# Kernel tuning notes

Hardware: AMD Instinct MI355X
Metric: run time of the kernel (lower is better)

The kernel has to match this reference:

```python
import jax, jax.numpy as jnp
import numpy as np

B, S, D = 1, 2048, 1024
HEADS, HEAD_DIM = 16, 64
GRID = (8, 16, 16)      # frames, height, width; prod == S
WIN = (3, 5, 5)         # window_f, window_h, window_w
NEG = -1e9


def _window_mask_3d(frames, height, width, wf, wh, ww):
    """[S, S] bool mask: True where kv is inside the 3D local window of q."""
    idx = np.arange(frames * height * width)
    f = idx // (height * width)
    hw = idx % (height * width)
    h = hw // width
    w = hw % width
    mf = np.abs(f[:, None] - f[None, :]) <= wf // 2
    mh = np.abs(h[:, None] - h[None, :]) <= wh // 2
    mw = np.abs(w[:, None] - w[None, :]) <= ww // 2
    return jnp.asarray(mf & mh & mw)


def setup_inputs() -> dict:
    key = jax.random.key(0)
    ks = jax.random.split(key, 6)
    sd = 1.0 / np.sqrt(D)
    return {
        "hidden_states": jax.random.normal(ks[0], (B, S, D), jnp.float32),
        "Wq": jax.random.normal(ks[1], (D, D), jnp.float32) * sd,
        "Wk": jax.random.normal(ks[2], (D, D), jnp.float32) * sd,
        "Wv": jax.random.normal(ks[3], (D, D), jnp.float32) * sd,
        "Wo": jax.random.normal(ks[4], (D, D), jnp.float32) * sd,
        "bo": jnp.zeros((D,), jnp.float32),
        "frames": GRID[0], "height": GRID[1], "width": GRID[2],
        "wf": WIN[0], "wh": WIN[1], "ww": WIN[2],
    }


def reference(hidden_states, Wq, Wk, Wv, Wo, bo, frames, height, width, wf, wh, ww):
    b, s, d = hidden_states.shape
    hd = d // HEADS
    scale = 1.0 / np.sqrt(hd)

    # QKV projections (attn.to_q / to_k / to_v, bias=False), self-attention
    q = (hidden_states @ Wq).reshape(b, s, HEADS, hd).transpose(0, 2, 1, 3)
    k = (hidden_states @ Wk).reshape(b, s, HEADS, hd).transpose(0, 2, 1, 3)
    v = (hidden_states @ Wv).reshape(b, s, HEADS, hd).transpose(0, 2, 1, 3)

    mask = _window_mask_3d(frames, height, width, wf, wh, ww)  # [S, S] bool

    # SDPA with boolean attn_mask (window-based block-sparse pattern)
    scores = jnp.einsum("bhqd,bhkd->bhqk", q, k) * scale
    scores = jnp.where(mask[None, None], scores, NEG)
    attnw = jax.nn.softmax(scores, axis=-1)
    out = jnp.einsum("bhqk,bhkd->bhqd", attnw, v)

    out = out.transpose(0, 2, 1, 3).reshape(b, s, d)
    return out @ Wo + bo
```

## Files before the change

kernel.cpp:

```cpp
#include <hip/hip_runtime.h>
#include <hip/hip_bf16.h>
#include <hip/hip_fp16.h>

#define SEQ   2048
#define DIM   1024
#define NHEAD 16
#define HD    64
#define QSCALE 0.18033688011112042f

typedef _Float16 half8 __attribute__((ext_vector_type(8)));
typedef _Float16 half4 __attribute__((ext_vector_type(4)));
typedef float    floatx4 __attribute__((ext_vector_type(4)));

__device__ __forceinline__ void gload16(const void* g, void* l) {
    __builtin_amdgcn_global_load_lds(
        (const __attribute__((address_space(1))) unsigned int*)g,
        (__attribute__((address_space(3))) unsigned int*)l, 16, 0, 0);
}

#define VMCNT(n) asm volatile("s_waitcnt vmcnt(" #n ")" ::: "memory")
#define BAR()    __builtin_amdgcn_s_barrier()

__global__ __launch_bounds__(256) void prep(
        const float* __restrict__ H, _Float16* __restrict__ Hf,
        const float* __restrict__ W0, const float* __restrict__ W1,
        const float* __restrict__ W2, const float* __restrict__ W3,
        _Float16* __restrict__ T) {
    __shared__ float tile[64][65];
    int z = blockIdx.z;
    int t = threadIdx.x;
    if (z < 4) {
        const float* W = (z == 0) ? W0 : (z == 1) ? W1 : (z == 2) ? W2 : W3;
        _Float16* Tz = T + (size_t)z * (DIM * DIM);
        int bx = blockIdx.x * 64;
        int by = blockIdx.y * 64;
        #pragma unroll
        for (int i = 0; i < 4; i++) {
            int id = t + i * 256;
            int r = id >> 4;
            int c = (id & 15) * 4;
            float4 v = *reinterpret_cast<const float4*>(W + (size_t)(by + r) * DIM + bx + c);
            tile[r][c] = v.x; tile[r][c + 1] = v.y; tile[r][c + 2] = v.z; tile[r][c + 3] = v.w;
        }
        __syncthreads();
        #pragma unroll
        for (int i = 0; i < 2; i++) {
            int id = t + i * 256;
            int nr = id >> 3;
            int c8 = id & 7;
            half8 o;
            #pragma unroll
            for (int j = 0; j < 8; j++) o[j] = (_Float16)tile[c8 * 8 + j][nr];
            *reinterpret_cast<half8*>(Tz + (size_t)(bx + nr) * DIM + by + c8 * 8) = o;
        }
    } else {
        int wg = blockIdx.y * 16 + blockIdx.x;
        #pragma unroll
        for (int i = 0; i < 4; i++) {
            int base = ((wg * 4 + i) * 256 + t) * 8;
            float4 v0 = *reinterpret_cast<const float4*>(H + base);
            float4 v1 = *reinterpret_cast<const float4*>(H + base + 4);
            half8 o = { (_Float16)v0.x, (_Float16)v0.y, (_Float16)v0.z, (_Float16)v0.w,
                        (_Float16)v1.x, (_Float16)v1.y, (_Float16)v1.z, (_Float16)v1.w };
            *reinterpret_cast<half8*>(Hf + base) = o;
        }
    }
}

__device__ __forceinline__ void gemm_core(const _Float16* __restrict__ Ap,
                                          const _Float16* __restrict__ Bp,
                                          char* lds, floatx4 (&acc)[4][4]) {
    const int tid  = threadIdx.x;
    const int lane = tid & 63;
    const int wid  = tid >> 6;
    const int wr = wid >> 1, wc = wid & 1;
    const int r16 = lane & 15;
    const int kk  = (lane >> 4) * 8;

    const int srow = tid >> 2, scol = (tid & 3) * 8;
    const _Float16* As0 = Ap + (size_t)srow * DIM + scol;
    const _Float16* Bs0 = Bp + (size_t)srow * DIM + scol;

    auto stage = [&](int buf, int t) {
        char* Ad = lds + buf * 32768;
        char* Bd = Ad + 16384;
        int k0 = t * 64;
        #pragma unroll
        for (int i = 0; i < 4; i++) {
            int off = (i & 1) * 64 * DIM + (i >> 1) * 32 + k0;
            gload16(As0 + off, Ad + i * 4096 + wid * 1024);
            gload16(Bs0 + off, Bd + i * 4096 + wid * 1024);
        }
    };

    auto compute = [&](int buf) {
        char* Ad = lds + buf * 32768;
        char* Bd = Ad + 16384;
        #pragma unroll
        for (int ks = 0; ks < 2; ks++) {
            half8 a[4], b[4];
            #pragma unroll
            for (int m = 0; m < 4; m++)
                a[m] = *reinterpret_cast<half8*>(Ad + ks * 8192 + (wr * 64 + m * 16 + r16) * 64 + kk * 2);
            #pragma unroll
            for (int n = 0; n < 4; n++)
                b[n] = *reinterpret_cast<half8*>(Bd + ks * 8192 + (wc * 64 + n * 16 + r16) * 64 + kk * 2);
            #pragma unroll
            for (int m = 0; m < 4; m++)
                #pragma unroll
                for (int n = 0; n < 4; n++)
                    acc[m][n] = __builtin_amdgcn_mfma_f32_16x16x32_f16(a[m], b[n], acc[m][n], 0, 0, 0);
        }
    };

    stage(0, 0);
    stage(1, 1);
    #pragma unroll 1
    for (int t = 0; t < 14; t += 2) {
        VMCNT(8); BAR();
        compute(0);
        BAR();
        stage(0, t + 2);
        VMCNT(8); BAR();
        compute(1);
        BAR();
        stage(1, t + 3);
    }
    VMCNT(8); BAR();
    compute(0);
    BAR();
    VMCNT(0); BAR();
    compute(1);
}

__global__ __launch_bounds__(256) void gemm_qkv(
        const _Float16* __restrict__ Hf, const _Float16* __restrict__ Wt,
        _Float16* __restrict__ Qp, _Float16* __restrict__ Kp, _Float16* __restrict__ Vt) {
    __shared__ char lds[65536];
    floatx4 acc[4][4] = {};

    int lin = blockIdx.x + 16 * blockIdx.y + 128 * blockIdx.z;
    int swz = (lin & 7) * 48 + (lin >> 3);
    int z  = swz >> 7;
    int rem = swz & 127;
    int bx = rem & 15, by = rem >> 4;

    int tm, tn;
    const _Float16 *Ap, *Bp;
    if (z < 2) {
        tm = bx; tn = by;
        Ap = Hf + (size_t)tm * 128 * DIM;
        Bp = Wt + (size_t)z * DIM * DIM + (size_t)tn * 128 * DIM;
    } else {
        tm = bx & 7; tn = by * 2 + (bx >> 3);
        Ap = Wt + (size_t)2 * DIM * DIM + (size_t)tm * 128 * DIM;
        Bp = Hf + (size_t)tn * 128 * DIM;
    }
    gemm_core(Ap, Bp, lds, acc);

    int lane = threadIdx.x & 63, wid = threadIdx.x >> 6;
    int wr = wid >> 1, wc = wid & 1;
    float qs = (z == 0) ? QSCALE : 1.0f;
    _Float16* Oz = (z == 0) ? Qp : Kp;

    #pragma unroll
    for (int m = 0; m < 4; m++) {
        #pragma unroll
        for (int n = 0; n < 4; n++) {
            #pragma unroll
            for (int r = 0; r < 4; r++) {
                int row = tm * 128 + wr * 64 + m * 16 + (lane >> 4) * 4 + r;
                int col = tn * 128 + wc * 64 + n * 16 + (lane & 15);
                float v = acc[m][n][r];
                if (z < 2) {
                    int head = col >> 6;
                    Oz[(size_t)head * (SEQ * HD) + (size_t)row * HD + (col & 63)] = (_Float16)(v * qs);
                } else {
                    Vt[(size_t)row * SEQ + col] = (_Float16)v;
                }
            }
        }
    }
}

__global__ __launch_bounds__(256) void gemm_o(
        const _Float16* __restrict__ AO, const _Float16* __restrict__ WoT,
        const float* __restrict__ bias, float* __restrict__ out) {
    __shared__ char lds[65536];
    floatx4 acc[4][4] = {};

    int lin = blockIdx.x + 16 * blockIdx.y;
    int swz = (lin & 7) * 16 + (lin >> 3);
    int tm = swz & 15, tn = swz >> 4;

    gemm_core(AO + (size_t)tm * 128 * DIM, WoT + (size_t)tn * 128 * DIM, lds, acc);

    int lane = threadIdx.x & 63, wid = threadIdx.x >> 6;
    int wr = wid >> 1, wc = wid & 1;
    #pragma unroll
    for (int m = 0; m < 4; m++) {
        #pragma unroll
        for (int n = 0; n < 4; n++) {
            #pragma unroll
            for (int r = 0; r < 4; r++) {
                int row = tm * 128 + wr * 64 + m * 16 + (lane >> 4) * 4 + r;
                int col = tn * 128 + wc * 64 + n * 16 + (lane & 15);
                out[(size_t)row * DIM + col] = acc[m][n][r] + bias[col];
            }
        }
    }
}

__global__ __launch_bounds__(256) void attn_mfma(
        const _Float16* __restrict__ Q,
        const _Float16* __restrict__ K,
        const _Float16* __restrict__ Vt,
        _Float16* __restrict__ AO) {
    __shared__ char P_lds[4][16 * 640];

    int wid  = threadIdx.x >> 6;
    int lane = threadIdx.x & 63;
    int g    = lane >> 4;
    int ql   = lane & 15;

    int blk  = blockIdx.x;
    int sblk = (blk & 7) * 64 + (blk >> 3);
    int bid  = sblk * 4 + wid;
    int rid  = bid & 127;
    int head = bid >> 7;
    int f    = rid >> 4;
    int hq   = rid & 15;
    int s0   = rid << 4;

    const _Float16* Qh = Q  + (size_t)head * (SEQ * HD);
    const _Float16* Kh = K  + (size_t)head * (SEQ * HD);
    const _Float16* Vh = Vt + (size_t)head * (HD * SEQ);

    int f_start = min(max(f - 1, 0), 5);
    int h_start = min(max(hq - 2, 0), 10);

    bool wm[4];
    #pragma unroll
    for (int r = 0; r < 4; r++) {
        int wp = g * 4 + r;
        wm[r] = (wp - ql <= 2) && (ql - wp <= 2);
    }

    half8 qf[2];
    #pragma unroll
    for (int ks = 0; ks < 2; ks++)
        qf[ks] = *reinterpret_cast<const half8*>(Qh + (size_t)(s0 + ql) * HD + ks * 32 + g * 8);

    float lsum = 0.f;
    int swz = (ql & 7) << 4;

    #pragma unroll
    for (int fi = 0; fi < 3; fi++) {
        int fp = f_start + fi;
        bool fok = (fp - f <= 1) && (f - fp <= 1);
        int sbase = fp * 256 + h_start * 16;
        const _Float16* Kc = Kh + (size_t)sbase * HD;

        floatx4 sacc[6];
        #pragma unroll
        for (int j = 0; j < 6; j++) sacc[j] = (floatx4){0.f, 0.f, 0.f, 0.f};

        #pragma unroll
        for (int j = 0; j < 6; j++) {
            #pragma unroll
            for (int ks = 0; ks < 2; ks++) {
                half8 kf = *reinterpret_cast<const half8*>(Kc + (size_t)(j * 16 + ql) * HD + ks * 32 + g * 8);
                sacc[j] = __builtin_amdgcn_mfma_f32_16x16x32_f16(kf, qf[ks], sacc[j], 0, 0, 0);
            }
        }

        #pragma unroll
        for (int j = 0; j < 6; j++) {
            int hp = h_start + j;
            bool ok = fok && (hp - hq <= 2) && (hq - hp <= 2);
            half4 pv;
            #pragma unroll
            for (int r = 0; r < 4; r++) {
                float sv = (ok && wm[r]) ? sacc[j][r] : -10000.f;
                float p  = __builtin_amdgcn_exp2f(sv);
                lsum += p;
                pv[r] = (_Float16)p;
            }
            int byte = (ql * 640 + (fi * 96 + j * 16 + g * 4) * 2) ^ swz;
            *reinterpret_cast<half4*>(&P_lds[wid][byte]) = pv;
        }
    }

    lsum += __shfl_xor(lsum, 16);
    lsum += __shfl_xor(lsum, 32);
    float inv = __builtin_amdgcn_rcpf(lsum);

    __syncthreads();

    floatx4 oacc[4];
    #pragma unroll
    for (int dt = 0; dt < 4; dt++) oacc[dt] = (floatx4){0.f, 0.f, 0.f, 0.f};

    #pragma unroll
    for (int fi = 0; fi < 3; fi++) {
        int sbase = (f_start + fi) * 256 + h_start * 16;
        #pragma unroll
        for (int kw = 0; kw < 3; kw++) {
            int kcol = fi * 96 + kw * 32;
            int byte = (ql * 640 + (kcol + g * 8) * 2) ^ swz;
            half8 pa = *reinterpret_cast<half8*>(&P_lds[wid][byte]);
            #pragma unroll
            for (int dt = 0; dt < 4; dt++) {
                half8 vf = *reinterpret_cast<const half8*>(
                    Vh + (size_t)(dt * 16 + ql) * SEQ + sbase + kw * 32 + g * 8);
                oacc[dt] = __builtin_amdgcn_mfma_f32_16x16x32_f16(pa, vf, oacc[dt], 0, 0, 0);
            }
        }
    }

    #pragma unroll
    for (int rr = 0; rr < 4; rr++) {
        float invr = __shfl(inv, g * 4 + rr);
        #pragma unroll
        for (int dt = 0; dt < 4; dt++) {
            AO[(size_t)(s0 + g * 4 + rr) * DIM + head * HD + dt * 16 + ql] =
                (_Float16)(oacc[dt][rr] * invr);
        }
    }
}

extern "C" void kernel_launch(void* const* d_in, const int* in_sizes, int n_in,
                              void* d_out, int out_size, void* d_ws, size_t ws_size,
                              hipStream_t stream) {
    const float* H  = (const float*)d_in[0];
    const float* Wq = (const float*)d_in[1];
    const float* Wk = (const float*)d_in[2];
    const float* Wv = (const float*)d_in[3];
    const float* Wo = (const float*)d_in[4];
    const float* bo = (const float*)d_in[5];

    char* ws = (char*)d_ws;
    _Float16* Hf = (_Float16*)(ws);
    _Float16* Wt = (_Float16*)(ws + (4u  << 20));
    _Float16* Qp = (_Float16*)(ws + (12u << 20));
    _Float16* Kp = (_Float16*)(ws + (16u << 20));
    _Float16* Vt = (_Float16*)(ws + (20u << 20));
    _Float16* AO = (_Float16*)(ws + (24u << 20));

    prep<<<dim3(16, 16, 5), 256, 0, stream>>>(H, Hf, Wq, Wk, Wv, Wo, Wt);

    gemm_qkv<<<dim3(16, 8, 3), 256, 0, stream>>>(Hf, Wt, Qp, Kp, Vt);

    attn_mfma<<<dim3(NHEAD * 128 / 4), 256, 0, stream>>>(Qp, Kp, Vt, AO);

    gemm_o<<<dim3(16, 8), 256, 0, stream>>>(AO, Wt + (size_t)3 * DIM * DIM, bo, (float*)d_out);
}
```

Baseline: 66.99 us.

## Use 128x64 tiles for output GEMM, relax attention barrier, add MFMA priority hints

The output projection GEMM switches to a new 128x64 tile core, launching 256 blocks instead of 128 so more of the GPU's compute units get work. Attention replaces a workgroup-wide barrier with an LDS-only wait, since each wave reads only its own P slice. It also raises wave priority around the MFMA loops. The smaller tiles reload more operand data and leave fewer MFMAs per LDS load. Dropping the barrier depends on each wave's P buffer being private, which the indexing by wave id suggests it is.

```diff
diff --git a/kernel.cpp b/kernel.cpp
--- a/kernel.cpp
+++ b/kernel.cpp
@@ -19,6 +19,7 @@
 }
 
 #define VMCNT(n) asm volatile("s_waitcnt vmcnt(" #n ")" ::: "memory")
+#define LGKM0()  asm volatile("s_waitcnt lgkmcnt(0)" ::: "memory")
 #define BAR()    __builtin_amdgcn_s_barrier()
 
 __global__ __launch_bounds__(256) void prep(
@@ -133,6 +134,74 @@
     compute(1);
 }
 
+__device__ __forceinline__ void gemm_core64(const _Float16* __restrict__ Ap,
+                                            const _Float16* __restrict__ Bp,
+                                            char* lds, floatx4 (&acc)[4][2]) {
+    const int tid  = threadIdx.x;
+    const int lane = tid & 63;
+    const int wid  = tid >> 6;
+    const int wr = wid >> 1, wc = wid & 1;
+    const int r16 = lane & 15;
+    const int kk  = (lane >> 4) * 8;
+
+    const int srow = tid >> 2, scol = (tid & 3) * 8;
+    const _Float16* As0 = Ap + (size_t)srow * DIM + scol;
+    const _Float16* Bs0 = Bp + (size_t)srow * DIM + scol;
+
+    auto stage = [&](int buf, int t) {
+        char* Ad = lds + buf * 24576;
+        char* Bd = Ad + 16384;
+        int k0 = t * 64;
+        #pragma unroll
+        for (int i = 0; i < 4; i++) {
+            int off = (i & 1) * 64 * DIM + (i >> 1) * 32 + k0;
+            gload16(As0 + off, Ad + i * 4096 + wid * 1024);
+        }
+        #pragma unroll
+        for (int j = 0; j < 2; j++)
+            gload16(Bs0 + j * 32 + k0, Bd + j * 4096 + wid * 1024);
+    };
+
+    auto compute = [&](int buf) {
+        char* Ad = lds + buf * 24576;
+        char* Bd = Ad + 16384;
+        #pragma unroll
+        for (int ks = 0; ks < 2; ks++) {
+            half8 a[4], b[2];
+            #pragma unroll
+            for (int m = 0; m < 4; m++)
+                a[m] = *reinterpret_cast<half8*>(Ad + ks * 8192 + (wr * 64 + m * 16 + r16) * 64 + kk * 2);
+            #pragma unroll
+            for (int n = 0; n < 2; n++)
+                b[n] = *reinterpret_cast<half8*>(Bd + ks * 4096 + (wc * 32 + n * 16 + r16) * 64 + kk * 2);
+            #pragma unroll
+            for (int m = 0; m < 4; m++)
+                #pragma unroll
+                for (int n = 0; n < 2; n++)
+                    acc[m][n] = __builtin_amdgcn_mfma_f32_16x16x32_f16(a[m], b[n], acc[m][n], 0, 0, 0);
+        }
+    };
+
+    stage(0, 0);
+    stage(1, 1);
+    #pragma unroll 1
+    for (int t = 0; t < 14; t += 2) {
+        VMCNT(6); BAR();
+        compute(0);
+        BAR();
+        stage(0, t + 2);
+        VMCNT(6); BAR();
+        compute(1);
+        BAR();
+        stage(1, t + 3);
+    }
+    VMCNT(6); BAR();
+    compute(0);
+    BAR();
+    VMCNT(0); BAR();
+    compute(1);
+}
+
 __global__ __launch_bounds__(256) void gemm_qkv(
         const _Float16* __restrict__ Hf, const _Float16* __restrict__ Wt,
         _Float16* __restrict__ Qp, _Float16* __restrict__ Kp, _Float16* __restrict__ Vt) {
@@ -186,25 +255,25 @@
 __global__ __launch_bounds__(256) void gemm_o(
         const _Float16* __restrict__ AO, const _Float16* __restrict__ WoT,
         const float* __restrict__ bias, float* __restrict__ out) {
-    __shared__ char lds[65536];
-    floatx4 acc[4][4] = {};
+    __shared__ char lds[49152];
+    floatx4 acc[4][2] = {};
 
     int lin = blockIdx.x + 16 * blockIdx.y;
-    int swz = (lin & 7) * 16 + (lin >> 3);
+    int swz = (lin & 7) * 32 + (lin >> 3);
     int tm = swz & 15, tn = swz >> 4;
 
-    gemm_core(AO + (size_t)tm * 128 * DIM, WoT + (size_t)tn * 128 * DIM, lds, acc);
+    gemm_core64(AO + (size_t)tm * 128 * DIM, WoT + (size_t)tn * 64 * DIM, lds, acc);
 
     int lane = threadIdx.x & 63, wid = threadIdx.x >> 6;
     int wr = wid >> 1, wc = wid & 1;
     #pragma unroll
     for (int m = 0; m < 4; m++) {
         #pragma unroll
-        for (int n = 0; n < 4; n++) {
+        for (int n = 0; n < 2; n++) {
             #pragma unroll
             for (int r = 0; r < 4; r++) {
                 int row = tm * 128 + wr * 64 + m * 16 + (lane >> 4) * 4 + r;
-                int col = tn * 128 + wc * 64 + n * 16 + (lane & 15);
+                int col = tn * 64 + wc * 32 + n * 16 + (lane & 15);
                 out[(size_t)row * DIM + col] = acc[m][n][r] + bias[col];
             }
         }
@@ -265,6 +334,7 @@
         #pragma unroll
         for (int j = 0; j < 6; j++) sacc[j] = (floatx4){0.f, 0.f, 0.f, 0.f};
 
+        __builtin_amdgcn_s_setprio(1);
         #pragma unroll
         for (int j = 0; j < 6; j++) {
             #pragma unroll
@@ -273,6 +343,7 @@
                 sacc[j] = __builtin_amdgcn_mfma_f32_16x16x32_f16(kf, qf[ks], sacc[j], 0, 0, 0);
             }
         }
+        __builtin_amdgcn_s_setprio(0);
 
         #pragma unroll
         for (int j = 0; j < 6; j++) {
@@ -295,7 +366,7 @@
     lsum += __shfl_xor(lsum, 32);
     float inv = __builtin_amdgcn_rcpf(lsum);
 
-    __syncthreads();
+    LGKM0();
 
     floatx4 oacc[4];
     #pragma unroll
@@ -304,6 +375,7 @@
     #pragma unroll
     for (int fi = 0; fi < 3; fi++) {
         int sbase = (f_start + fi) * 256 + h_start * 16;
+        __builtin_amdgcn_s_setprio(1);
         #pragma unroll
         for (int kw = 0; kw < 3; kw++) {
             int kcol = fi * 96 + kw * 32;
@@ -316,6 +388,7 @@
                 oacc[dt] = __builtin_amdgcn_mfma_f32_16x16x32_f16(pa, vf, oacc[dt], 0, 0, 0);
             }
         }
+        __builtin_amdgcn_s_setprio(0);
     }
 
     #pragma unroll
@@ -353,5 +426,5 @@
 
     attn_mfma<<<dim3(NHEAD * 128 / 4), 256, 0, stream>>>(Qp, Kp, Vt, AO);
 
-    gemm_o<<<dim3(16, 8), 256, 0, stream>>>(AO, Wt + (size_t)3 * DIM * DIM, bo, (float*)d_out);
-}
+    gemm_o<<<dim3(16, 16), 256, 0, stream>>>(AO, Wt + (size_t)3 * DIM * DIM, bo, (float*)d_out);
+}
```

Result: faster. 59.97 us (-10.5%).
